# Optimization experiments

Measured on AMD Instinct MI355X. Metric: run time of the kernel, lower is better.

## Reference

```python
import jax, jax.numpy as jnp
import numpy as np

B, S, E = 32, 128, 128
NQ, NS = 100000, 512
QN, SN = 4, 10
S_MAX = 4
NEG = -1e30


def setup_inputs() -> dict:
    key = jax.random.key(0)
    ks = jax.random.split(key, 24)
    def nrm(k, shape, sc):
        return jax.random.normal(k, shape, jnp.float32) * sc
    inp = {}
    inp['question'] = jax.random.randint(ks[0], (B, S), 0, NQ, jnp.int32)
    inp['response'] = jax.random.randint(ks[1], (B, S), 0, 2, jnp.int32)
    inp['mask'] = jax.random.randint(ks[2], (B, S), 0, 2, jnp.int32)
    inp['q_neighbors'] = jax.random.randint(ks[3], (NQ, QN), 0, NS, jnp.int32)
    inp['s_neighbors'] = jax.random.randint(ks[4], (NS, SN), 0, NQ, jnp.int32)
    sidx = jax.random.randint(ks[5], (NQ, S_MAX), 0, NS, jnp.int32)
    inp['qs_table'] = jnp.zeros((NQ, NS), jnp.float32).at[jnp.arange(NQ)[:, None], sidx].set(1.0)
    inp['emb_q'] = nrm(ks[6], (NQ, E), 1.0)
    inp['emb_s'] = nrm(ks[7], (NS, E), 1.0)
    inp['emb_r'] = nrm(ks[8], (2, E), 1.0)
    s_in = 1.0 / np.sqrt(2 * E).astype(np.float32)
    s_e = 1.0 / np.sqrt(E).astype(np.float32)
    inp['W_ih'] = nrm(ks[9], (4 * E, 2 * E), s_in)
    inp['b_ih'] = nrm(ks[10], (4 * E,), s_in)
    inp['b_hh'] = nrm(ks[11], (4 * E,), s_in)
    inp['W_agg'] = nrm(ks[12], (3, E, E), s_e)
    inp['b_agg'] = nrm(ks[13], (3, E), s_e)
    inp['W_last'] = nrm(ks[14], (E, E), s_e)
    inp['b_last'] = nrm(ks[15], (E,), s_e)
    inp['W_query'] = nrm(ks[16], (E, E), s_e)
    inp['b_query'] = nrm(ks[17], (E,), s_e)
    inp['W_key'] = nrm(ks[18], (E, E), s_e)
    inp['b_key'] = nrm(ks[19], (E,), s_e)
    inp['w_W'] = nrm(ks[20], (2 * E,), s_in)
    inp['b_W'] = nrm(ks[21], (), s_in)
    return inp


def _forward(question, response, mask, q_neighbors, s_neighbors, qs_table,
             emb_q, emb_s, emb_r, W_ih, b_ih, b_hh, W_agg, b_agg, W_last, b_last,
             W_query, b_query, W_key, b_key, w_W, b_W):
    Bq, Sq = question.shape
    Ed = emb_q.shape[1]
    AGG = W_agg.shape[0]
    w_q, w_k = w_W[:Ed], w_W[Ed:]
    c_pad = jnp.tanh(b_query) @ w_k  # attention logit piece of an all-zero padded state
    pos = jnp.arange(Sq)

    def step(state_history, xs):
        t, q_t, r_t, m_t, q_next = xs
        # ---- multi-hop neighbor gather (q -> s -> q -> s) ----
        n1 = q_neighbors[q_t]              # [B,QN] skill ids
        n2 = s_neighbors[n1]               # [B,QN,SN] question ids
        n3 = q_neighbors[n2]               # [B,QN,SN,QN] skill ids
        e = [emb_q[q_t], emb_s[n1], emb_q[n2], emb_s[n3]]
        # triangular mean-aggregate (dropout is identity in eval mode)
        for i in range(AGG):
            for j in range(AGG - i):
                e[j] = jnp.tanh((e[j + 1].mean(-2) + e[j]) @ W_agg[j].T + b_agg[j])
        agg = jnp.tanh(e[0] @ W_last.T + b_last)
        emb_qt = jnp.where((m_t == 1)[:, None], agg, emb_q[q_t])
        # ---- LSTMCell with zero initial (h, c): W_hh @ 0 drops out, b_hh remains ----
        x = jnp.concatenate([emb_qt, emb_r[r_t]], -1)
        gates = x @ W_ih.T + b_ih + b_hh
        gi, gf, gg, go = jnp.split(gates, 4, -1)
        h = jax.nn.sigmoid(go) * jnp.tanh(jax.nn.sigmoid(gi) * jnp.tanh(gg))
        # ---- skills related to next question; zero-padded rows contribute exactly 0 ----
        vals, sidx = jax.lax.top_k(qs_table[q_next], S_MAX)
        emb_sk = emb_s[sidx] * (vals > 0.0)[..., None]
        qs_concat = jnp.concatenate([emb_q[q_next][:, None], emb_sk], 1)  # [B,1+S_MAX,E]
        # ---- hard recap: history steps whose question is a 2-hop neighbor of q_next ----
        q_rel = s_neighbors[q_neighbors[q_next]].reshape(Bq, -1)          # [B,QN*SN]
        matches = (question[:, :, None] == q_rel[:, None, :]).any(-1) & (pos[None, :] < t)
        n_sel = matches.sum(-1)
        P = (jnp.max(n_sel) - n_sel).astype(jnp.float32)  # zero-pad count to per-batch max
        # ---- predict: MLP_W(concat(Q,K)) is rank-1 => logit = a[b,q] + c[b,s] ----
        a = jnp.tanh(qs_concat @ W_key.T + b_key) @ w_q + b_W             # [B,Qd]
        c_hist = jnp.tanh(state_history @ W_query.T + b_query) @ w_k      # [B,S]
        c_cur = jnp.tanh(h @ W_query.T + b_query) @ w_k                   # [B]
        lh = jnp.where(matches[:, None, :], a[:, :, None] + c_hist[:, None, :], NEG)
        lc = a + c_cur[:, None]
        lp = a + c_pad
        m = jnp.maximum(jnp.maximum(lh.max(-1), lc), lp)
        Eh = jnp.exp(lh - m[:, :, None])
        Ec = jnp.exp(lc - m)
        Ep = jnp.exp(lp - m)
        g_hist = jnp.einsum('bqe,bse->bqs', qs_concat, state_history)
        g_cur = jnp.einsum('bqe,be->bq', qs_concat, h)
        denom = Eh.sum(-1) + Ec + P[:, None] * Ep  # zero-pad states counted analytically
        num = (Eh * g_hist).sum(-1) + Ec * g_cur   # pads multiply g=0 -> no numerator term
        y = jax.nn.sigmoid(jnp.sum(num / denom, axis=1))
        # original skips the state write at t == 0 (slot 0 stays zero forever)
        state_history = state_history.at[:, t].set(jnp.where(t > 0, h, jnp.zeros_like(h)))
        return state_history, y

    ts = jnp.arange(Sq - 1)
    xs = (ts, question[:, :-1].T, response[:, :-1].T, mask[:, :-1].T, question[:, 1:].T)
    init = jnp.zeros((Bq, Sq, Ed), jnp.float32)
    _, ys = jax.lax.scan(step, init, xs)
    return jnp.zeros((Bq, Sq), jnp.float32).at[:, 0].set(0.5).at[:, 1:].set(ys.T)


def reference(question, response, mask, q_neighbors, s_neighbors, qs_table,
              emb_q, emb_s, emb_r, W_ih, b_ih, b_hh, W_agg, b_agg, W_last, b_last,
              W_query, b_query, W_key, b_key, w_W, b_W):
    return _forward(question, response, mask, q_neighbors, s_neighbors, qs_table,
                    emb_q, emb_s, emb_r, W_ih, b_ih, b_hh, W_agg, b_agg, W_last, b_last,
                    W_query, b_query, W_key, b_key, w_W, b_W)
```

## Files before the change

### kernel.cpp

```cpp
#include <hip/hip_runtime.h>
#include <stdint.h>

#define NB 32
#define SEQ 128
#define EMB 128
#define NSTEP 127
#define NS 512

__device__ __forceinline__ float ftanh(float x){ float e=__expf(2.f*x); return 1.f-2.f/(e+1.f); }
__device__ __forceinline__ float fsig(float x){ return 1.f/(1.f+__expf(-x)); }
__device__ __forceinline__ float4 ld4(const float* p){ return *(const float4*)p; }

#define FMA4(acc, xv, a0, a1, a2, a3) \
  acc.x = fmaf(xv.x, a0.x, fmaf(xv.y, a1.x, fmaf(xv.z, a2.x, fmaf(xv.w, a3.x, acc.x)))); \
  acc.y = fmaf(xv.x, a0.y, fmaf(xv.y, a1.y, fmaf(xv.z, a2.y, fmaf(xv.w, a3.y, acc.y)))); \
  acc.z = fmaf(xv.x, a0.z, fmaf(xv.y, a1.z, fmaf(xv.z, a2.z, fmaf(xv.w, a3.z, acc.z)))); \
  acc.w = fmaf(xv.x, a0.w, fmaf(xv.y, a1.w, fmaf(xv.z, a2.w, fmaf(xv.w, a3.w, acc.w))));

template<int K, int XS>
__device__ __forceinline__ void gemm8(const float* __restrict__ WT, int NEtot,
                                      const float* Xl, const float* __restrict__ bias,
                                      float* outb)
{
  const int tid = threadIdx.x;
  const int et = tid & 31;
  const int rt = tid >> 5;
  const float* wp = WT + et*4;
  const float* xr = Xl + rt*XS;
  constexpr int G = K/4;
  float4 acc = {0.f,0.f,0.f,0.f};
  float4 w0 = ld4(wp);
  float4 w1 = ld4(wp + NEtot);
  float4 w2 = ld4(wp + 2*NEtot);
  float4 w3 = ld4(wp + 3*NEtot);
  const float* wq = wp + (size_t)4*NEtot;
  float4 m0 = ld4(wq);
  float4 m1 = ld4(wq + NEtot);
  float4 m2 = ld4(wq + 2*NEtot);
  float4 m3 = ld4(wq + 3*NEtot);
  #pragma unroll 2
  for (int g = 0; g + 2 < G; g += 2) {
    const float* wa = wp + (size_t)(4*(g+2))*NEtot;
    float4 n0 = ld4(wa);
    float4 n1 = ld4(wa + NEtot);
    float4 n2 = ld4(wa + 2*NEtot);
    float4 n3 = ld4(wa + 3*NEtot);
    float4 xa = ld4(xr + 4*g);
    FMA4(acc, xa, w0, w1, w2, w3);
    w0=n0; w1=n1; w2=n2; w3=n3;
    const float* wb = wp + (size_t)(4*(g+3))*NEtot;
    float4 o0 = ld4(wb);
    float4 o1 = ld4(wb + NEtot);
    float4 o2 = ld4(wb + 2*NEtot);
    float4 o3 = ld4(wb + 3*NEtot);
    float4 xb = ld4(xr + 4*(g+1));
    FMA4(acc, xb, m0, m1, m2, m3);
    m0=o0; m1=o1; m2=o2; m3=o3;
  }
  {
    float4 xa = ld4(xr + 4*(G-2));
    FMA4(acc, xa, w0, w1, w2, w3);
    float4 xb = ld4(xr + 4*(G-1));
    FMA4(acc, xb, m0, m1, m2, m3);
  }
  float4 bb = ld4(bias + et*4);
  acc.x+=bb.x; acc.y+=bb.y; acc.z+=bb.z; acc.w+=bb.w;
  *(float4*)(outb + rt*132 + et*4) = acc;
}

template<int K, int XS>
__device__ __forceinline__ void gemm2(const float* __restrict__ WT, int NEtot,
                                      const float* Xl, const float* __restrict__ bias,
                                      float* outb)
{
  const int tid = threadIdx.x;
  const int et = tid & 31;
  const int rt = tid >> 5;
  const float* wp = WT + et*4;
  const float* xr = Xl + (size_t)(rt*2)*XS;
  constexpr int G = K/4;
  float4 a0 = {0.f,0.f,0.f,0.f};
  float4 a1 = {0.f,0.f,0.f,0.f};
  float4 w0 = ld4(wp);
  float4 w1 = ld4(wp + NEtot);
  float4 w2 = ld4(wp + 2*NEtot);
  float4 w3 = ld4(wp + 3*NEtot);
  const float* wq = wp + (size_t)4*NEtot;
  float4 m0 = ld4(wq);
  float4 m1 = ld4(wq + NEtot);
  float4 m2 = ld4(wq + 2*NEtot);
  float4 m3 = ld4(wq + 3*NEtot);
  #pragma unroll 2
  for (int g = 0; g + 2 < G; g += 2) {
    const float* wa = wp + (size_t)(4*(g+2))*NEtot;
    float4 n0 = ld4(wa);
    float4 n1 = ld4(wa + NEtot);
    float4 n2 = ld4(wa + 2*NEtot);
    float4 n3 = ld4(wa + 3*NEtot);
    float4 xa0 = ld4(xr + 4*g);
    float4 xa1 = ld4(xr + XS + 4*g);
    FMA4(a0, xa0, w0, w1, w2, w3);
    FMA4(a1, xa1, w0, w1, w2, w3);
    w0=n0; w1=n1; w2=n2; w3=n3;
    const float* wb = wp + (size_t)(4*(g+3))*NEtot;
    float4 o0 = ld4(wb);
    float4 o1 = ld4(wb + NEtot);
    float4 o2 = ld4(wb + 2*NEtot);
    float4 o3 = ld4(wb + 3*NEtot);
    float4 xb0 = ld4(xr + 4*(g+1));
    float4 xb1 = ld4(xr + XS + 4*(g+1));
    FMA4(a0, xb0, m0, m1, m2, m3);
    FMA4(a1, xb1, m0, m1, m2, m3);
    m0=o0; m1=o1; m2=o2; m3=o3;
  }
  {
    float4 xa0 = ld4(xr + 4*(G-2));
    float4 xa1 = ld4(xr + XS + 4*(G-2));
    FMA4(a0, xa0, w0, w1, w2, w3);
    FMA4(a1, xa1, w0, w1, w2, w3);
    float4 xb0 = ld4(xr + 4*(G-1));
    float4 xb1 = ld4(xr + XS + 4*(G-1));
    FMA4(a0, xb0, m0, m1, m2, m3);
    FMA4(a1, xb1, m0, m1, m2, m3);
  }
  float4 bb = ld4(bias + et*4);
  a0.x+=bb.x; a0.y+=bb.y; a0.z+=bb.z; a0.w+=bb.w;
  a1.x+=bb.x; a1.y+=bb.y; a1.z+=bb.z; a1.w+=bb.w;
  float* ob = outb + (size_t)(rt*2)*132 + et*4;
  *(float4*)(ob)       = a0;
  *(float4*)(ob + 132) = a1;
}

__global__ __launch_bounds__(256) void k_T(
    const float* __restrict__ W_agg, const float* __restrict__ W_last,
    const float* __restrict__ W_query, const float* __restrict__ W_ih,
    const float* __restrict__ b_ih, const float* __restrict__ b_hh,
    const float* __restrict__ b_query, const float* __restrict__ w_W,
    float* __restrict__ WT012, float* __restrict__ WLT, float* __restrict__ WQT,
    float* __restrict__ WIHT, float* __restrict__ BIH, float* __restrict__ CPAD,
    float* __restrict__ G1, int* __restrict__ Pmaxi)
{
  const int gid = blockIdx.x*256 + threadIdx.x;
  const int gsz = gridDim.x*256;
  for (int i = gid; i < 49152; i += gsz) {
    int j = i >> 14, rem = i & 16383, k = rem >> 7, e = rem & 127;
    WT012[i] = W_agg[j*16384 + e*128 + k];
  }
  for (int i = gid; i < 16384; i += gsz) {
    int k = i >> 7, e = i & 127;
    WLT[i] = W_last[e*128 + k];
    WQT[i] = W_query[e*128 + k];
  }
  for (int i = gid; i < 131072; i += gsz) {
    int k = i >> 9, e = i & 511;
    WIHT[i] = W_ih[e*256 + k];
  }
  for (int i = gid; i < 65536; i += gsz) G1[i] = 0.f;
  if (gid < 512) BIH[gid] = b_ih[gid] + b_hh[gid];
  if (gid < 128) Pmaxi[gid] = 0;
  if (blockIdx.x == 0) {
    __shared__ float red[256];
    float v = (threadIdx.x < 128) ? ftanh(b_query[threadIdx.x]) * w_W[128 + threadIdx.x] : 0.f;
    red[threadIdx.x] = v; __syncthreads();
    #pragma unroll
    for (int s = 128; s > 0; s >>= 1) {
      if (threadIdx.x < s) red[threadIdx.x] += red[threadIdx.x + s];
      __syncthreads();
    }
    if (threadIdx.x == 0) CPAD[0] = red[0];
  }
}

__global__ __launch_bounds__(128) void k_pre(
    const int* __restrict__ s_neighbors, const int* __restrict__ q_neighbors,
    const float* __restrict__ emb_q, const float* __restrict__ emb_s,
    const float* __restrict__ WT012, const float* __restrict__ b_agg,
    float* __restrict__ E1, float* __restrict__ G1)
{
  __shared__ float XA[4*132];
  __shared__ float XB[4*132];
  __shared__ int idx[40];
  __shared__ int n3[16];
  const int tid = threadIdx.x;
  const int blk = blockIdx.x;
  if (blk < 128) {
    const int s0 = blk*4;
    if (tid < 40) idx[tid] = s_neighbors[s0*10 + tid];
    __syncthreads();
    {
      int r = tid >> 5, e4 = (tid & 31) << 2;
      float4 a = ld4(emb_s + (size_t)(s0+r)*128 + e4);
      float sx=0,sy=0,sz=0,sw=0;
      #pragma unroll
      for (int jj = 0; jj < 10; ++jj) {
        float4 q = ld4(emb_q + (size_t)idx[r*10+jj]*128 + e4);
        sx+=q.x; sy+=q.y; sz+=q.z; sw+=q.w;
      }
      float4 o; o.x=a.x+0.1f*sx; o.y=a.y+0.1f*sy; o.z=a.z+0.1f*sz; o.w=a.w+0.1f*sw;
      *(float4*)(XA + r*132 + e4) = o;
    }
    __syncthreads();
    gemm8<128,132>(WT012 + 16384, 128, XA, b_agg + 128, XB);
    __syncthreads();
    for (int f = tid; f < 512; f += 128) {
      int r = f >> 7, e = f & 127;
      E1[(size_t)(s0+r)*128 + e] = ftanh(XB[r*132 + e]);
    }
  } else {
    const int p0 = (blk-128)*4;
    if (tid < 4) idx[tid] = s_neighbors[p0 + tid];
    __syncthreads();
    if (tid < 16) n3[tid] = q_neighbors[(size_t)idx[tid>>2]*4 + (tid&3)];
    __syncthreads();
    {
      int r = tid >> 5, e4 = (tid & 31) << 2;
      float4 a = ld4(emb_q + (size_t)idx[r]*128 + e4);
      float sx=0,sy=0,sz=0,sw=0;
      #pragma unroll
      for (int k = 0; k < 4; ++k) {
        float4 q = ld4(emb_s + (size_t)n3[r*4+k]*128 + e4);
        sx+=q.x; sy+=q.y; sz+=q.z; sw+=q.w;
      }
      float4 o; o.x=a.x+0.25f*sx; o.y=a.y+0.25f*sy; o.z=a.z+0.25f*sz; o.w=a.w+0.25f*sw;
      *(float4*)(XA + r*132 + e4) = o;
    }
    __syncthreads();
    gemm8<128,132>(WT012 + 32768, 128, XA, b_agg + 256, XB);
    __syncthreads();
    for (int f = tid; f < 512; f += 128) {
      int r = f >> 7, e = f & 127;
      atomicAdd(&G1[(size_t)((p0+r)/10)*128 + e], ftanh(XB[r*132 + e]));
    }
  }
}

__global__ __launch_bounds__(128) void k_pre2(
    const float* __restrict__ E1, const float* __restrict__ G1,
    const float* __restrict__ WT012, const float* __restrict__ b_agg,
    float* __restrict__ E2)
{
  __shared__ float XA[4*132];
  __shared__ float XB[4*132];
  const int tid = threadIdx.x;
  const int s0 = blockIdx.x*4;
  for (int f = tid; f < 512; f += 128) {
    int r = f >> 7, e = f & 127;
    XA[r*132 + e] = 0.1f*G1[(size_t)(s0+r)*128 + e] + E1[(size_t)(s0+r)*128 + e];
  }
  __syncthreads();
  gemm8<128,132>(WT012 + 16384, 128, XA, b_agg + 128, XB);
  __syncthreads();
  for (int f = tid; f < 512; f += 128) {
    int r = f >> 7, e = f & 127;
    E2[(size_t)(s0+r)*128 + e] = ftanh(XB[r*132 + e]);
  }
}

__global__ __launch_bounds__(256) void k_chain(
    const int* __restrict__ question, const int* __restrict__ response,
    const int* __restrict__ maskp, const int* __restrict__ q_neighbors,
    const int* __restrict__ s_neighbors,
    const float* __restrict__ emb_q, const float* __restrict__ emb_s,
    const float* __restrict__ emb_r,
    const float* __restrict__ WT012, const float* __restrict__ WLT,
    const float* __restrict__ WQT, const float* __restrict__ WIHT,
    const float* __restrict__ BIH,
    const float* __restrict__ b_agg, const float* __restrict__ b_last,
    const float* __restrict__ b_query, const float* __restrict__ w_W,
    const float* __restrict__ E1, const float* __restrict__ E2,
    float* __restrict__ Hfull, float* __restrict__ Cq,
    int* __restrict__ nsel, unsigned long long* __restrict__ mwords,
    int* __restrict__ Pmaxi)
{
  __shared__ float XA[16*132];
  __shared__ float XB[16*132];
  __shared__ float M1[16*132];
  __shared__ float M2[16*132];
  __shared__ float XC[16*264];
  __shared__ int qts[16], rts[16], mts[16], n1s[64];

  const int tid = threadIdx.x;
  const int blk = blockIdx.x;

  if (tid < 16) {
    int rid = blk*16 + tid;
    int b = rid / 127, t = rid - b*127;
    qts[tid] = question[b*SEQ + t];
    rts[tid] = response[b*SEQ + t];
    mts[tid] = maskp[b*SEQ + t];
  }
  __syncthreads();
  if (tid < 64) n1s[tid] = q_neighbors[(size_t)qts[tid>>2]*4 + (tid&3)];
  __syncthreads();
  {
    const int e4 = (tid & 31) << 2;
    for (int rr = tid >> 5; rr < 16; rr += 8) {
      const int* nn = n1s + rr*4;
      float4 a = ld4(emb_q + (size_t)qts[rr]*128 + e4);
      float s1x=0,s1y=0,s1z=0,s1w=0, s2x=0,s2y=0,s2z=0,s2w=0, s3x=0,s3y=0,s3z=0,s3w=0;
      #pragma unroll
      for (int i = 0; i < 4; ++i) {
        float4 q1 = ld4(emb_s + (size_t)nn[i]*128 + e4);
        float4 q2 = ld4(E1 + (size_t)nn[i]*128 + e4);
        float4 q3 = ld4(E2 + (size_t)nn[i]*128 + e4);
        s1x+=q1.x; s1y+=q1.y; s1z+=q1.z; s1w+=q1.w;
        s2x+=q2.x; s2y+=q2.y; s2z+=q2.z; s2w+=q2.w;
        s3x+=q3.x; s3y+=q3.y; s3z+=q3.z; s3w+=q3.w;
      }
      float4 o; o.x=a.x+0.25f*s1x; o.y=a.y+0.25f*s1y; o.z=a.z+0.25f*s1z; o.w=a.w+0.25f*s1w;
      *(float4*)(XA + rr*132 + e4) = o;
      float4 p; p.x=0.25f*s2x; p.y=0.25f*s2y; p.z=0.25f*s2z; p.w=0.25f*s2w;
      *(float4*)(M1 + rr*132 + e4) = p;
      float4 u; u.x=0.25f*s3x; u.y=0.25f*s3y; u.z=0.25f*s3z; u.w=0.25f*s3w;
      *(float4*)(M2 + rr*132 + e4) = u;
    }
  }
  __syncthreads();
  gemm2<128,132>(WT012, 128, XA, b_agg, XB);
  __syncthreads();
  for (int f = tid; f < 2112; f += 256) XB[f] = M1[f] + ftanh(XB[f]);
  __syncthreads();
  gemm2<128,132>(WT012, 128, XB, b_agg, XA);
  __syncthreads();
  for (int f = tid; f < 2112; f += 256) XA[f] = M2[f] + ftanh(XA[f]);
  __syncthreads();
  gemm2<128,132>(WT012, 128, XA, b_agg, XB);
  __syncthreads();
  for (int f = tid; f < 2112; f += 256) XB[f] = ftanh(XB[f]);
  __syncthreads();
  gemm2<128,132>(WLT, 128, XB, b_last, XA);
  __syncthreads();
  for (int f = tid; f < 2048; f += 256) {
    int r = f >> 7, e = f & 127;
    float agg = ftanh(XA[r*132 + e]);
    XC[r*264 + e] = (mts[r] == 1) ? agg : emb_q[(size_t)qts[r]*128 + e];
    XC[r*264 + 128 + e] = emb_r[rts[r]*128 + e];
  }
  __syncthreads();
  gemm2<256,264>(WIHT,       512, XC, BIH,       XA);
  gemm2<256,264>(WIHT + 256, 512, XC, BIH + 256, XB);
  gemm2<256,264>(WIHT + 384, 512, XC, BIH + 384, M1);
  __syncthreads();
  for (int f = tid; f < 2048; f += 256) {
    int r = f >> 7, e = f & 127;
    float gi = XA[r*132 + e], gg = XB[r*132 + e], go = M1[r*132 + e];
    float h = fsig(go) * ftanh(fsig(gi) * ftanh(gg));
    XC[r*264 + e] = h;
    Hfull[(size_t)(blk*16 + r)*128 + e] = h;
  }
  __syncthreads();
  gemm2<128,264>(WQT, 128, XC, b_query, XA);
  __syncthreads();
  {
    const int et = tid & 31, rt = tid >> 5;
    float4 wv = ld4(w_W + 128 + et*4);
    for (int rr = rt; rr < 16; rr += 8) {
      float4 o = ld4(XA + rr*132 + et*4);
      float s = ftanh(o.x)*wv.x + ftanh(o.y)*wv.y + ftanh(o.z)*wv.z + ftanh(o.w)*wv.w;
      #pragma unroll
      for (int off = 16; off > 0; off >>= 1) s += __shfl_down(s, off);
      if (et == 0) Cq[blk*16 + rr] = s;
    }
  }
  {
    const int wv = tid >> 6;
    const int ln = tid & 63;
    for (int rr = wv; rr < 16; rr += 4) {
      int rid = blk*16 + rr;
      int b = rid / 127, t = rid - b*127;
      int q_next = question[b*SEQ + t + 1];
      int qrv = 0;
      if (ln < 40)
        qrv = s_neighbors[(size_t)q_neighbors[(size_t)q_next*4 + ln/10]*10 + ln%10];
      int q0 = question[b*SEQ + ln];
      int q1 = question[b*SEQ + 64 + ln];
      bool p0 = false, p1 = false;
      #pragma unroll 8
      for (int i = 0; i < 40; ++i) {
        int qv = __shfl(qrv, i);
        p0 |= (q0 == qv); p1 |= (q1 == qv);
      }
      p0 &= (ln < t);
      p1 &= (64 + ln < t);
      unsigned long long w0 = __ballot(p0);
      unsigned long long w1 = __ballot(p1);
      if (ln == 0) {
        size_t bt = (size_t)b*NSTEP + t;
        mwords[bt*2 + 0] = w0;
        mwords[bt*2 + 1] = w1;
        int ns = __popcll(w0) + __popcll(w1);
        nsel[bt] = ns;
        atomicMax(&Pmaxi[t], ns);
      }
    }
  }
}

__device__ __forceinline__ float wredsum(float v) {
  #pragma unroll
  for (int o = 32; o > 0; o >>= 1) v += __shfl_down(v, o);
  return v;
}
__device__ __forceinline__ float wredmax(float v) {
  #pragma unroll
  for (int o = 32; o > 0; o >>= 1) v = fmaxf(v, __shfl_down(v, o));
  return v;
}

__global__ __launch_bounds__(128) void k_attn(
    const int* __restrict__ question, const float* __restrict__ qs_table,
    const float* __restrict__ emb_q, const float* __restrict__ emb_s,
    const float* __restrict__ CPAD,
    const float* __restrict__ Hfull, const float* __restrict__ Cq,
    const int* __restrict__ nsel, const unsigned long long* __restrict__ mwords,
    const int* __restrict__ Pmaxi, float* __restrict__ out)
{
  __shared__ float us[128];
  __shared__ int cols[8];
  __shared__ int cnt;
  __shared__ float smx[2];
  __shared__ float s3[2][3];
  const int tid = threadIdx.x;
  const int wid = tid >> 6;
  const int bid = blockIdx.x;
  const int b = bid / NSTEP, t = bid % NSTEP;
  const size_t bt = (size_t)b*NSTEP + t;
  const int q_next = question[b*SEQ + t + 1];

  if (tid == 0) cnt = 0;
  __syncthreads();
  {
    float4 v = ld4(qs_table + (size_t)q_next*NS + tid*4);
    if (v.x > 0.f) { int p = atomicAdd(&cnt, 1); if (p < 8) cols[p] = tid*4; }
    if (v.y > 0.f) { int p = atomicAdd(&cnt, 1); if (p < 8) cols[p] = tid*4+1; }
    if (v.z > 0.f) { int p = atomicAdd(&cnt, 1); if (p < 8) cols[p] = tid*4+2; }
    if (v.w > 0.f) { int p = atomicAdd(&cnt, 1); if (p < 8) cols[p] = tid*4+3; }
  }
  __syncthreads();
  const int nc = min(cnt, 4);
  {
    float ue = emb_q[(size_t)q_next*EMB + tid];
    for (int i = 0; i < nc; ++i) ue += emb_s[(size_t)cols[i]*EMB + tid];
    us[tid] = ue;
  }
  const float c_pad = CPAD[0];
  const float P = (float)(Pmaxi[t] - nsel[bt]);

  const unsigned long long w0 = mwords[bt*2 + 0];
  const unsigned long long w1 = mwords[bt*2 + 1];
  const bool matched = (tid < 64) ? ((w0 >> tid) & 1ull)
                                  : ((w1 >> (tid - 64)) & 1ull);
  const float c_cur = Cq[bt];
  float Cp = matched ? ((tid == 0) ? c_pad : Cq[(size_t)b*NSTEP + tid]) : -3.0e38f;
  float mh = wredmax(Cp);
  if ((tid & 63) == 0) smx[wid] = mh;
  __syncthreads();
  float M = fmaxf(fmaxf(smx[0], smx[1]), fmaxf(c_cur, c_pad));
  float wgt = matched ? __expf(Cp - M) : 0.f;
  float dotp = 0.f;
  if (matched && tid >= 1) {
    const float* hp = Hfull + ((size_t)b*NSTEP + tid)*EMB;
    float s = 0.f;
    #pragma unroll 8
    for (int e = 0; e < 128; e += 4) {
      float4 h4 = ld4(hp + e);
      s = fmaf(us[e],h4.x, fmaf(us[e+1],h4.y, fmaf(us[e+2],h4.z, fmaf(us[e+3],h4.w, s))));
    }
    dotp = s;
  }
  float gcp = us[tid] * Hfull[bt*EMB + tid];
  float a0 = wredsum(wgt);
  float a1 = wredsum(wgt * dotp);
  float a2 = wredsum(gcp);
  if ((tid & 63) == 0) { s3[wid][0] = a0; s3[wid][1] = a1; s3[wid][2] = a2; }
  __syncthreads();
  if (tid == 0) {
    float Sexp = s3[0][0] + s3[1][0];
    float Snum = s3[0][1] + s3[1][1];
    float gc   = s3[0][2] + s3[1][2];
    float Ec = __expf(c_cur - M), Ep = __expf(c_pad - M);
    float D = Sexp + Ec + P * Ep;
    float numt = Snum + Ec * gc;
    out[b*SEQ + t + 1] = fsig(numt / D);
    if (t == 0) out[b*SEQ] = 0.5f;
  }
}

extern "C" void kernel_launch(void* const* d_in, const int* in_sizes, int n_in,
                              void* d_out, int out_size, void* d_ws, size_t ws_size,
                              hipStream_t stream) {
  const int* question    = (const int*)d_in[0];
  const int* response    = (const int*)d_in[1];
  const int* maskp       = (const int*)d_in[2];
  const int* q_neighbors = (const int*)d_in[3];
  const int* s_neighbors = (const int*)d_in[4];
  const float* qs_table  = (const float*)d_in[5];
  const float* emb_q     = (const float*)d_in[6];
  const float* emb_s     = (const float*)d_in[7];
  const float* emb_r     = (const float*)d_in[8];
  const float* W_ih      = (const float*)d_in[9];
  const float* b_ih      = (const float*)d_in[10];
  const float* b_hh      = (const float*)d_in[11];
  const float* W_agg     = (const float*)d_in[12];
  const float* b_agg     = (const float*)d_in[13];
  const float* W_last    = (const float*)d_in[14];
  const float* b_last    = (const float*)d_in[15];
  const float* W_query   = (const float*)d_in[16];
  const float* b_query   = (const float*)d_in[17];
  const float* w_W       = (const float*)d_in[20];
  float* out = (float*)d_out;

  float* ws = (float*)d_ws;
  float* WT012 = ws;
  float* WLT   = ws + 49152;
  float* WQT   = ws + 65536;
  float* WIHT  = ws + 81920;
  float* BIH   = ws + 212992;
  float* CPAD  = ws + 213504;
  float* E1    = ws + 213520;
  float* G1    = ws + 279056;
  float* E2    = ws + 344592;
  float* Hfull = ws + 410128;
  float* Cq    = ws + 930320;
  int*   Pmaxi = (int*)(ws + 934384);
  int*   nselp = (int*)(ws + 934512);
  unsigned long long* mwords =
      (unsigned long long*)(((uintptr_t)(ws + 938576) + 15) & ~(uintptr_t)15);

  k_T<<<dim3(512), dim3(256), 0, stream>>>(
      W_agg, W_last, W_query, W_ih, b_ih, b_hh, b_query, w_W,
      WT012, WLT, WQT, WIHT, BIH, CPAD, G1, Pmaxi);
  k_pre<<<dim3(1408), dim3(128), 0, stream>>>(
      s_neighbors, q_neighbors, emb_q, emb_s, WT012, b_agg, E1, G1);
  k_pre2<<<dim3(128), dim3(128), 0, stream>>>(E1, G1, WT012, b_agg, E2);
  k_chain<<<dim3(254), dim3(256), 0, stream>>>(
      question, response, maskp, q_neighbors, s_neighbors, emb_q, emb_s, emb_r,
      WT012, WLT, WQT, WIHT, BIH, b_agg, b_last, b_query, w_W,
      E1, E2, Hfull, Cq, nselp, mwords, Pmaxi);
  k_attn<<<dim3(NB*NSTEP), dim3(128), 0, stream>>>(
      question, qs_table, emb_q, emb_s, CPAD, Hfull, Cq,
      nselp, mwords, Pmaxi, out);
}
```

Before: 399.1 us.

## Split K dimension across two thread halves in k_chain GEMMs, use 512 threads

Doubles k_chain's block size to 512 threads and splits each GEMM's reduction dimension in half. The second half writes partial sums to a new shared buffer, PB, which the following elementwise pass adds back in. This is meant to shorten the serial per-block chain of small GEMMs, since the grid has only 254 blocks and the GPU is underfilled. In exchange it adds shared-memory traffic and extra sync/add passes, especially for the three LSTM gate GEMMs, which are now serialized with a barrier after each.

After: 392.7 us. Within noise of the previous version (-1.6%).

```diff
diff --git a/kernel.cpp b/kernel.cpp
--- a/kernel.cpp
+++ b/kernel.cpp
@@ -69,16 +69,18 @@
 }
 
 template<int K, int XS>
-__device__ __forceinline__ void gemm2(const float* __restrict__ WT, int NEtot,
-                                      const float* Xl, const float* __restrict__ bias,
-                                      float* outb)
+__device__ __forceinline__ void gemmKS(const float* __restrict__ WT, int NEtot,
+                                       const float* Xl, const float* __restrict__ bias,
+                                       float* outb, float* partb)
 {
   const int tid = threadIdx.x;
   const int et = tid & 31;
-  const int rt = tid >> 5;
-  const float* wp = WT + et*4;
-  const float* xr = Xl + (size_t)(rt*2)*XS;
-  constexpr int G = K/4;
+  const int kt = (tid >> 5) & 1;
+  const int rg = tid >> 6;
+  constexpr int KH = K/2;
+  constexpr int G  = KH/4;
+  const float* wp = WT + (size_t)kt*KH*NEtot + et*4;
+  const float* xr = Xl + (size_t)(rg*2)*XS + kt*KH;
   float4 a0 = {0.f,0.f,0.f,0.f};
   float4 a1 = {0.f,0.f,0.f,0.f};
   float4 w0 = ld4(wp);
@@ -123,10 +125,16 @@
     FMA4(a0, xb0, m0, m1, m2, m3);
     FMA4(a1, xb1, m0, m1, m2, m3);
   }
-  float4 bb = ld4(bias + et*4);
-  a0.x+=bb.x; a0.y+=bb.y; a0.z+=bb.z; a0.w+=bb.w;
-  a1.x+=bb.x; a1.y+=bb.y; a1.z+=bb.z; a1.w+=bb.w;
-  float* ob = outb + (size_t)(rt*2)*132 + et*4;
+  float* dst;
+  if (kt == 0) {
+    float4 bb = ld4(bias + et*4);
+    a0.x+=bb.x; a0.y+=bb.y; a0.z+=bb.z; a0.w+=bb.w;
+    a1.x+=bb.x; a1.y+=bb.y; a1.z+=bb.z; a1.w+=bb.w;
+    dst = outb;
+  } else {
+    dst = partb;
+  }
+  float* ob = dst + (size_t)(rg*2)*132 + et*4;
   *(float4*)(ob)       = a0;
   *(float4*)(ob + 132) = a1;
 }
@@ -256,7 +264,7 @@
   }
 }
 
-__global__ __launch_bounds__(256) void k_chain(
+__global__ __launch_bounds__(512) void k_chain(
     const int* __restrict__ question, const int* __restrict__ response,
     const int* __restrict__ maskp, const int* __restrict__ q_neighbors,
     const int* __restrict__ s_neighbors,
@@ -276,6 +284,7 @@
   __shared__ float XB[16*132];
   __shared__ float M1[16*132];
   __shared__ float M2[16*132];
+  __shared__ float PB[16*132];
   __shared__ float XC[16*264];
   __shared__ int qts[16], rts[16], mts[16], n1s[64];
 
@@ -294,78 +303,98 @@
   __syncthreads();
   {
     const int e4 = (tid & 31) << 2;
-    for (int rr = tid >> 5; rr < 16; rr += 8) {
-      const int* nn = n1s + rr*4;
-      float4 a = ld4(emb_q + (size_t)qts[rr]*128 + e4);
-      float s1x=0,s1y=0,s1z=0,s1w=0, s2x=0,s2y=0,s2z=0,s2w=0, s3x=0,s3y=0,s3z=0,s3w=0;
-      #pragma unroll
-      for (int i = 0; i < 4; ++i) {
-        float4 q1 = ld4(emb_s + (size_t)nn[i]*128 + e4);
-        float4 q2 = ld4(E1 + (size_t)nn[i]*128 + e4);
-        float4 q3 = ld4(E2 + (size_t)nn[i]*128 + e4);
-        s1x+=q1.x; s1y+=q1.y; s1z+=q1.z; s1w+=q1.w;
-        s2x+=q2.x; s2y+=q2.y; s2z+=q2.z; s2w+=q2.w;
-        s3x+=q3.x; s3y+=q3.y; s3z+=q3.z; s3w+=q3.w;
-      }
-      float4 o; o.x=a.x+0.25f*s1x; o.y=a.y+0.25f*s1y; o.z=a.z+0.25f*s1z; o.w=a.w+0.25f*s1w;
-      *(float4*)(XA + rr*132 + e4) = o;
-      float4 p; p.x=0.25f*s2x; p.y=0.25f*s2y; p.z=0.25f*s2z; p.w=0.25f*s2w;
-      *(float4*)(M1 + rr*132 + e4) = p;
-      float4 u; u.x=0.25f*s3x; u.y=0.25f*s3y; u.z=0.25f*s3z; u.w=0.25f*s3w;
-      *(float4*)(M2 + rr*132 + e4) = u;
-    }
-  }
-  __syncthreads();
-  gemm2<128,132>(WT012, 128, XA, b_agg, XB);
-  __syncthreads();
-  for (int f = tid; f < 2112; f += 256) XB[f] = M1[f] + ftanh(XB[f]);
-  __syncthreads();
-  gemm2<128,132>(WT012, 128, XB, b_agg, XA);
-  __syncthreads();
-  for (int f = tid; f < 2112; f += 256) XA[f] = M2[f] + ftanh(XA[f]);
-  __syncthreads();
-  gemm2<128,132>(WT012, 128, XA, b_agg, XB);
-  __syncthreads();
-  for (int f = tid; f < 2112; f += 256) XB[f] = ftanh(XB[f]);
-  __syncthreads();
-  gemm2<128,132>(WLT, 128, XB, b_last, XA);
-  __syncthreads();
-  for (int f = tid; f < 2048; f += 256) {
-    int r = f >> 7, e = f & 127;
-    float agg = ftanh(XA[r*132 + e]);
+    const int rr = tid >> 5;
+    const int* nn = n1s + rr*4;
+    float4 a = ld4(emb_q + (size_t)qts[rr]*128 + e4);
+    float s1x=0,s1y=0,s1z=0,s1w=0, s2x=0,s2y=0,s2z=0,s2w=0, s3x=0,s3y=0,s3z=0,s3w=0;
+    #pragma unroll
+    for (int i = 0; i < 4; ++i) {
+      float4 q1 = ld4(emb_s + (size_t)nn[i]*128 + e4);
+      float4 q2 = ld4(E1 + (size_t)nn[i]*128 + e4);
+      float4 q3 = ld4(E2 + (size_t)nn[i]*128 + e4);
+      s1x+=q1.x; s1y+=q1.y; s1z+=q1.z; s1w+=q1.w;
+      s2x+=q2.x; s2y+=q2.y; s2z+=q2.z; s2w+=q2.w;
+      s3x+=q3.x; s3y+=q3.y; s3z+=q3.z; s3w+=q3.w;
+    }
+    float4 o; o.x=a.x+0.25f*s1x; o.y=a.y+0.25f*s1y; o.z=a.z+0.25f*s1z; o.w=a.w+0.25f*s1w;
+    *(float4*)(XA + rr*132 + e4) = o;
+    float4 p; p.x=0.25f*s2x; p.y=0.25f*s2y; p.z=0.25f*s2z; p.w=0.25f*s2w;
+    *(float4*)(M1 + rr*132 + e4) = p;
+    float4 u; u.x=0.25f*s3x; u.y=0.25f*s3y; u.z=0.25f*s3z; u.w=0.25f*s3w;
+    *(float4*)(M2 + rr*132 + e4) = u;
+  }
+  __syncthreads();
+  gemmKS<128,132>(WT012, 128, XA, b_agg, XB, PB);
+  __syncthreads();
+  for (int f = tid; f < 2048; f += 512) {
+    int i = (f >> 7)*132 + (f & 127);
+    XB[i] = M1[i] + ftanh(XB[i] + PB[i]);
+  }
+  __syncthreads();
+  gemmKS<128,132>(WT012, 128, XB, b_agg, XA, PB);
+  __syncthreads();
+  for (int f = tid; f < 2048; f += 512) {
+    int i = (f >> 7)*132 + (f & 127);
+    XA[i] = M2[i] + ftanh(XA[i] + PB[i]);
+  }
+  __syncthreads();
+  gemmKS<128,132>(WT012, 128, XA, b_agg, XB, PB);
+  __syncthreads();
+  for (int f = tid; f < 2048; f += 512) {
+    int i = (f >> 7)*132 + (f & 127);
+    XB[i] = ftanh(XB[i] + PB[i]);
+  }
+  __syncthreads();
+  gemmKS<128,132>(WLT, 128, XB, b_last, XA, PB);
+  __syncthreads();
+  for (int f = tid; f < 2048; f += 512) {
+    int r = f >> 7, e = f & 127, i = r*132 + e;
+    float agg = ftanh(XA[i] + PB[i]);
     XC[r*264 + e] = (mts[r] == 1) ? agg : emb_q[(size_t)qts[r]*128 + e];
     XC[r*264 + 128 + e] = emb_r[rts[r]*128 + e];
   }
   __syncthreads();
-  gemm2<256,264>(WIHT,       512, XC, BIH,       XA);
-  gemm2<256,264>(WIHT + 256, 512, XC, BIH + 256, XB);
-  gemm2<256,264>(WIHT + 384, 512, XC, BIH + 384, M1);
-  __syncthreads();
-  for (int f = tid; f < 2048; f += 256) {
-    int r = f >> 7, e = f & 127;
-    float gi = XA[r*132 + e], gg = XB[r*132 + e], go = M1[r*132 + e];
+  gemmKS<256,264>(WIHT,       512, XC, BIH,       XA, PB);
+  __syncthreads();
+  for (int f = tid; f < 2048; f += 512) {
+    int i = (f >> 7)*132 + (f & 127);
+    XA[i] += PB[i];
+  }
+  __syncthreads();
+  gemmKS<256,264>(WIHT + 256, 512, XC, BIH + 256, XB, PB);
+  __syncthreads();
+  for (int f = tid; f < 2048; f += 512) {
+    int i = (f >> 7)*132 + (f & 127);
+    XB[i] += PB[i];
+  }
+  __syncthreads();
+  gemmKS<256,264>(WIHT + 384, 512, XC, BIH + 384, M1, PB);
+  __syncthreads();
+  for (int f = tid; f < 2048; f += 512) {
+    int r = f >> 7, e = f & 127, i = r*132 + e;
+    float gi = XA[i], gg = XB[i], go = M1[i] + PB[i];
     float h = fsig(go) * ftanh(fsig(gi) * ftanh(gg));
     XC[r*264 + e] = h;
     Hfull[(size_t)(blk*16 + r)*128 + e] = h;
   }
   __syncthreads();
-  gemm2<128,264>(WQT, 128, XC, b_query, XA);
-  __syncthreads();
-  {
-    const int et = tid & 31, rt = tid >> 5;
+  gemmKS<128,264>(WQT, 128, XC, b_query, XA, PB);
+  __syncthreads();
+  {
+    const int et = tid & 31, rr = tid >> 5;
     float4 wv = ld4(w_W + 128 + et*4);
-    for (int rr = rt; rr < 16; rr += 8) {
-      float4 o = ld4(XA + rr*132 + et*4);
-      float s = ftanh(o.x)*wv.x + ftanh(o.y)*wv.y + ftanh(o.z)*wv.z + ftanh(o.w)*wv.w;
-      #pragma unroll
-      for (int off = 16; off > 0; off >>= 1) s += __shfl_down(s, off);
-      if (et == 0) Cq[blk*16 + rr] = s;
-    }
+    float4 o = ld4(XA + rr*132 + et*4);
+    float4 p = ld4(PB + rr*132 + et*4);
+    float s = ftanh(o.x+p.x)*wv.x + ftanh(o.y+p.y)*wv.y
+            + ftanh(o.z+p.z)*wv.z + ftanh(o.w+p.w)*wv.w;
+    #pragma unroll
+    for (int off = 16; off > 0; off >>= 1) s += __shfl_down(s, off);
+    if (et == 0) Cq[blk*16 + rr] = s;
   }
   {
     const int wv = tid >> 6;
     const int ln = tid & 63;
-    for (int rr = wv; rr < 16; rr += 4) {
+    for (int rr = wv; rr < 16; rr += 8) {
       int rid = blk*16 + rr;
       int b = rid / 127, t = rid - b*127;
       int q_next = question[b*SEQ + t + 1];
@@ -533,7 +562,7 @@
   k_pre<<<dim3(1408), dim3(128), 0, stream>>>(
       s_neighbors, q_neighbors, emb_q, emb_s, WT012, b_agg, E1, G1);
   k_pre2<<<dim3(128), dim3(128), 0, stream>>>(E1, G1, WT012, b_agg, E2);
-  k_chain<<<dim3(254), dim3(256), 0, stream>>>(
+  k_chain<<<dim3(254), dim3(512), 0, stream>>>(
       question, response, maskp, q_neighbors, s_neighbors, emb_q, emb_s, emb_r,
       WT012, WLT, WQT, WIHT, BIH, b_agg, b_last, b_query, w_W,
       E1, E2, Hfull, Cq, nselp, mwords, Pmaxi);
```
